# Kernel optimization log

Measured on AMD Instinct MI355X. Metric: run time of the kernel, lower is better.

## Reference

```python
import jax, jax.numpy as jnp
import numpy as np

EMBD = 256
HEAD = 4
HD = EMBD // HEAD  # 64
EPS = 1e-5


def setup_inputs() -> dict:
    key = jax.random.key(0)
    ks = jax.random.split(key, 12)
    s = lambda fan_in: 1.0 / np.sqrt(fan_in)
    return {
        "x": jax.random.normal(ks[0], (16, 1024, EMBD), dtype=jnp.float32),
        # attention params (stored as [in, out])
        "qkv_w": jax.random.uniform(ks[1], (EMBD, 3 * EMBD), jnp.float32, -s(EMBD), s(EMBD)),
        "qkv_b": jax.random.uniform(ks[2], (3 * EMBD,), jnp.float32, -s(EMBD), s(EMBD)),
        "out_w": jax.random.uniform(ks[3], (EMBD, EMBD), jnp.float32, -s(EMBD), s(EMBD)),
        "out_b": jax.random.uniform(ks[4], (EMBD,), jnp.float32, -s(EMBD), s(EMBD)),
        # MLP params
        "fc_w": jax.random.uniform(ks[5], (EMBD, 4 * EMBD), jnp.float32, -s(EMBD), s(EMBD)),
        "fc_b": jax.random.uniform(ks[6], (4 * EMBD,), jnp.float32, -s(EMBD), s(EMBD)),
        "proj_w": jax.random.uniform(ks[7], (4 * EMBD, EMBD), jnp.float32, -s(4 * EMBD), s(4 * EMBD)),
        "proj_b": jax.random.uniform(ks[8], (EMBD,), jnp.float32, -s(4 * EMBD), s(4 * EMBD)),
        # LayerNorm params
        "ln1_g": jnp.ones((EMBD,), jnp.float32),
        "ln1_b": jnp.zeros((EMBD,), jnp.float32),
        "ln2_g": jnp.ones((EMBD,), jnp.float32),
        "ln2_b": jnp.zeros((EMBD,), jnp.float32),
    }


def layer_norm(x, g, b):
    mu = jnp.mean(x, axis=-1, keepdims=True)
    var = jnp.mean(jnp.square(x - mu), axis=-1, keepdims=True)
    return (x - mu) * jax.lax.rsqrt(var + EPS) * g + b


def block_forward(x, qkv_w, qkv_b, out_w, out_b, fc_w, fc_b, proj_w, proj_b,
                  ln1_g, ln1_b, ln2_g, ln2_b):
    B, S, E = x.shape
    # --- attention branch ---
    h = layer_norm(x, ln1_g, ln1_b)
    qkv = h @ qkv_w + qkv_b                       # [B,S,3E]
    q, k, v = jnp.split(qkv, 3, axis=-1)
    q = q.reshape(B, S, HEAD, HD).transpose(0, 2, 1, 3)  # [B,H,S,D]
    k = k.reshape(B, S, HEAD, HD).transpose(0, 2, 1, 3)
    v = v.reshape(B, S, HEAD, HD).transpose(0, 2, 1, 3)
    att = jnp.einsum('bhqd,bhkd->bhqk', q, k) / jnp.sqrt(jnp.float32(HD))
    causal = jnp.tril(jnp.ones((S, S), dtype=bool))
    att = jnp.where(causal, att, -jnp.inf)
    att = jax.nn.softmax(att, axis=-1)
    o = jnp.einsum('bhqk,bhkd->bhqd', att, v)     # [B,H,S,D]
    o = o.transpose(0, 2, 1, 3).reshape(B, S, E)
    x = x + o @ out_w + out_b
    # --- MLP branch (dropout inactive at eval) ---
    h = layer_norm(x, ln2_g, ln2_b)
    h = jax.nn.relu(h @ fc_w + fc_b)
    x = x + h @ proj_w + proj_b
    return x


def reference(x, qkv_w, qkv_b, out_w, out_b, fc_w, fc_b, proj_w, proj_b,
              ln1_g, ln1_b, ln2_g, ln2_b):
    return block_forward(x, qkv_w, qkv_b, out_w, out_b, fc_w, fc_b,
                         proj_w, proj_b, ln1_g, ln1_b, ln2_g, ln2_b)
```

## Files before the change

### kernel.cpp

```cpp
#include <hip/hip_runtime.h>
#include <cstdint>


using f32x4  = __attribute__((ext_vector_type(4))) float;
using f32x16 = __attribute__((ext_vector_type(16))) float;
using s16x8  = __attribute__((ext_vector_type(8))) short;
using s16x4  = __attribute__((ext_vector_type(4))) short;

__device__ inline short f2bf(float f) {
    union { float f; unsigned u; } v{f};
    unsigned r = (v.u + 0x7FFFu + ((v.u >> 16) & 1u)) >> 16;
    return (short)r;
}

__device__ inline int cvt_pk_bf16(float lo, float hi) {
    int d;
    asm("v_cvt_pk_bf16_f32 %0, %1, %2" : "=v"(d) : "v"(lo), "v"(hi));
    return d;
}
__device__ inline void swap32(int& a, int& b) {
    asm("v_permlane32_swap_b32 %0, %1" : "+v"(a), "+v"(b));
}
__device__ inline void swap16(int& a, int& b) {
    asm("v_permlane16_swap_b32 %0, %1" : "+v"(a), "+v"(b));
}

__device__ inline void gload16(const void* g, void* l) {
    __builtin_amdgcn_global_load_lds(
        (const __attribute__((address_space(1))) void*)g,
        (__attribute__((address_space(3))) void*)l, 16, 0, 0);
}

__global__ __launch_bounds__(256) void prep_kernel(
    const float* __restrict__ qkv_w, const float* __restrict__ out_w,
    const float* __restrict__ fc_w,  const float* __restrict__ proj_w,
    short* __restrict__ wt_qkv, short* __restrict__ wt_out,
    short* __restrict__ wt_fc,  short* __restrict__ wt_proj,
    const float* __restrict__ x, const float* __restrict__ ln1_g,
    const float* __restrict__ ln1_b, short* __restrict__ hout)
{
    __shared__ short T[64][65];
    int id  = blockIdx.x;
    int tid = threadIdx.x;

    if (id < 192) {
        const float* W; short* Wt; int K, N, nt, kt;
        if (id < 48)       { W = qkv_w;  Wt = wt_qkv;  K = 256;  N = 768;  nt = id % 12;        kt = id / 12; }
        else if (id < 64)  { W = out_w;  Wt = wt_out;  K = 256;  N = 256;  nt = (id - 48) & 3;  kt = (id - 48) >> 2; }
        else if (id < 128) { W = fc_w;   Wt = wt_fc;   K = 256;  N = 1024; nt = (id - 64) & 15; kt = (id - 64) >> 4; }
        else               { W = proj_w; Wt = wt_proj; K = 1024; N = 256;  nt = (id - 128) & 3; kt = (id - 128) >> 2; }
        int n0 = nt * 64, k0 = kt * 64;
        int r = tid >> 2, c = (tid & 3) << 4;
        const float* src = W + (size_t)(k0 + r) * N + n0 + c;
#pragma unroll
        for (int u = 0; u < 4; ++u) {
            float4 v = *reinterpret_cast<const float4*>(src + u * 4);
            T[r][c + u * 4 + 0] = f2bf(v.x);
            T[r][c + u * 4 + 1] = f2bf(v.y);
            T[r][c + u * 4 + 2] = f2bf(v.z);
            T[r][c + u * 4 + 3] = f2bf(v.w);
        }
        __syncthreads();
        s16x8 o0, o1;
#pragma unroll
        for (int jj = 0; jj < 8; ++jj) { o0[jj] = T[c + jj][r]; o1[jj] = T[c + 8 + jj][r]; }
        short* dst = Wt + (size_t)(n0 + r) * K + k0 + c;
        *reinterpret_cast<s16x8*>(dst)     = o0;
        *reinterpret_cast<s16x8*>(dst + 8) = o1;
    } else {
        int lane = tid & 63;
        int row  = (id - 192) * 4 + (tid >> 6);
        const float* xr = x + (size_t)row * 256;
        float4 v = *reinterpret_cast<const float4*>(xr + lane * 4);
        float s = v.x + v.y + v.z + v.w;
#pragma unroll
        for (int o2 = 32; o2 >= 1; o2 >>= 1) s += __shfl_xor(s, o2);
        float mu = s * (1.0f / 256.0f);
        float dx = v.x - mu, dy = v.y - mu, dz = v.z - mu, dw = v.w - mu;
        float q = dx * dx + dy * dy + dz * dz + dw * dw;
#pragma unroll
        for (int o2 = 32; o2 >= 1; o2 >>= 1) q += __shfl_xor(q, o2);
        float rstd = rsqrtf(q * (1.0f / 256.0f) + 1e-5f);
        float4 gv = *reinterpret_cast<const float4*>(ln1_g + lane * 4);
        float4 bv = *reinterpret_cast<const float4*>(ln1_b + lane * 4);
        s16x4 ov;
        ov[0] = f2bf(dx * rstd * gv.x + bv.x);
        ov[1] = f2bf(dy * rstd * gv.y + bv.y);
        ov[2] = f2bf(dz * rstd * gv.z + bv.z);
        ov[3] = f2bf(dw * rstd * gv.w + bv.w);
        *reinterpret_cast<s16x4*>(hout + (size_t)row * 256 + lane * 4) = ov;
    }
}

template <int BM>
__global__ __launch_bounds__(256) void qkv_gemm_kernel(const short* __restrict__ A,
                                                       const short* __restrict__ Bt,
                                                       const float* __restrict__ bias,
                                                       short* __restrict__ qkout,
                                                       short* __restrict__ vt,
                                                       int N, int K)
{
    constexpr int MI = BM / 32;
    __shared__ short As[BM * 64];
    __shared__ short Bs[128 * 64];

    int tid = threadIdx.x;
    int l   = tid & 63;
    int w   = tid >> 6;
    int lr  = l & 15;
    int lk8 = (l >> 4) << 3;
    int r4  = (l >> 4) << 2;
    int wr  = w >> 1, wc = w & 1;
    int bn  = blockIdx.x * 128, bm = blockIdx.y * BM;

    int scolS = ((l & 7) << 3) ^ ((l >> 3) << 3);
    int srowA = w * (BM / 4) + (l >> 3);
    int srowB = (w << 5) + (l >> 3);
    const short* pa = A  + (size_t)(bm + srowA) * K + scolS;
    const short* pb = Bt + (size_t)(bn + srowB) * K + scolS;
    short* dstA = As + w * (BM / 4) * 64;
    short* dstB = Bs + (w << 11);

    f32x4 acc[MI][4];
#pragma unroll
    for (int mi = 0; mi < MI; ++mi)
#pragma unroll
        for (int ni = 0; ni < 4; ++ni) acc[mi][ni] = (f32x4){0.f, 0.f, 0.f, 0.f};

    int swz = (lr & 7) << 3;

    for (int k0 = 0; k0 < K; k0 += 64) {
        __syncthreads();
#pragma unroll
        for (int i = 0; i < BM / 32; ++i)
            gload16(pa + (size_t)(i * 8) * K + k0, dstA + (i << 9));
#pragma unroll
        for (int i = 0; i < 4; ++i)
            gload16(pb + (size_t)(i * 8) * K + k0, dstB + (i << 9));
        __syncthreads();

#pragma unroll
        for (int ks = 0; ks < 2; ++ks) {
            s16x8 af[MI], bf[4];
#pragma unroll
            for (int mi = 0; mi < MI; ++mi) {
                int row = wr * (BM / 2) + (mi << 4) + lr;
                af[mi] = *reinterpret_cast<const s16x8*>(
                    &As[(row << 6) + (((ks << 5) + lk8) ^ swz)]);
            }
#pragma unroll
            for (int ni = 0; ni < 4; ++ni) {
                int row = (wc << 6) + (ni << 4) + lr;
                bf[ni] = *reinterpret_cast<const s16x8*>(
                    &Bs[(row << 6) + (((ks << 5) + lk8) ^ swz)]);
            }
            __builtin_amdgcn_s_setprio(1);
#pragma unroll
            for (int mi = 0; mi < MI; ++mi)
#pragma unroll
                for (int ni = 0; ni < 4; ++ni)
                    acc[mi][ni] = __builtin_amdgcn_mfma_f32_16x16x32_bf16(
                        af[mi], bf[ni], acc[mi][ni], 0, 0, 0);
            __builtin_amdgcn_s_setprio(0);
        }
    }

    float bv[4];
#pragma unroll
    for (int ni = 0; ni < 4; ++ni)
        bv[ni] = bias[bn + (wc << 6) + (ni << 4) + lr];

#pragma unroll
    for (int mi = 0; mi < MI; ++mi) {
#pragma unroll
        for (int ni = 0; ni < 4; ++ni) {
            int n = bn + (wc << 6) + (ni << 4) + lr;
#pragma unroll
            for (int r = 0; r < 4; ++r) {
                int m = bm + wr * (BM / 2) + (mi << 4) + r4 + r;
                float v = acc[mi][ni][r] + bv[ni];
                if (bn < 512) {
                    qkout[(size_t)m * 512 + n] = f2bf(v);
                } else {
                    int hh = (n - 512) >> 6, dd = (n - 512) & 63;
                    int bb = m >> 10, ss = m & 1023;
                    vt[(size_t)((((bb << 2) | hh) << 6) | dd) * 1024 + ss] = f2bf(v);
                }
            }
        }
    }
}

__global__ __launch_bounds__(256) void oproj_ln_kernel(const short* __restrict__ A,
                                                       const short* __restrict__ Bt,
                                                       const float* __restrict__ bias,
                                                       const float* __restrict__ R,
                                                       float* __restrict__ x1,
                                                       short* __restrict__ h2,
                                                       const float* __restrict__ g,
                                                       const float* __restrict__ bb)
{
    constexpr int ASZ = 64 * 64;
    constexpr int BSZ = 256 * 64;
    __shared__ short As[2 * ASZ];
    __shared__ short Bs[2 * BSZ];

    int tid = threadIdx.x;
    int l   = tid & 63;
    int w   = tid >> 6;
    int lr  = l & 15;
    int lk8 = (l >> 4) << 3;
    int r4  = (l >> 4) << 2;
    int bm  = blockIdx.x * 64;

    int scolS = ((l & 7) << 3) ^ ((l >> 3) << 3);
    const short* pa = A  + (size_t)(bm + (w << 4) + (l >> 3)) * 256 + scolS;
    const short* pb = Bt + (size_t)((w << 6) + (l >> 3)) * 256 + scolS;
    short* dstA = As + (w << 10);
    short* dstB = Bs + (w << 12);

    f32x4 acc[16];
#pragma unroll
    for (int ni = 0; ni < 16; ++ni) acc[ni] = (f32x4){0.f, 0.f, 0.f, 0.f};

    int swz = (lr & 7) << 3;

#pragma unroll
    for (int i = 0; i < 2; ++i)
        gload16(pa + (size_t)(i * 8) * 256, dstA + (i << 9));
#pragma unroll
    for (int i = 0; i < 8; ++i)
        gload16(pb + (size_t)(i * 8) * 256, dstB + (i << 9));
    __syncthreads();

    int cur = 0;
    for (int k0 = 0; k0 < 256; k0 += 64) {
        if (k0 + 64 < 256) {
            int nxt = cur ^ 1;
#pragma unroll
            for (int i = 0; i < 2; ++i)
                gload16(pa + (size_t)(i * 8) * 256 + k0 + 64, dstA + nxt * ASZ + (i << 9));
#pragma unroll
            for (int i = 0; i < 8; ++i)
                gload16(pb + (size_t)(i * 8) * 256 + k0 + 64, dstB + nxt * BSZ + (i << 9));
        }
        const short* curA = As + cur * ASZ;
        const short* curB = Bs + cur * BSZ;
#pragma unroll
        for (int ks = 0; ks < 2; ++ks) {
            int arow = (w << 4) + lr;
            s16x8 af = *reinterpret_cast<const s16x8*>(
                &curA[(arow << 6) + (((ks << 5) + lk8) ^ swz)]);
            __builtin_amdgcn_s_setprio(1);
#pragma unroll
            for (int ni = 0; ni < 16; ++ni) {
                int row = (ni << 4) + lr;
                s16x8 bf = *reinterpret_cast<const s16x8*>(
                    &curB[(row << 6) + (((ks << 5) + lk8) ^ swz)]);
                acc[ni] = __builtin_amdgcn_mfma_f32_16x16x32_bf16(af, bf, acc[ni], 0, 0, 0);
            }
            __builtin_amdgcn_s_setprio(0);
        }
        __syncthreads();
        cur ^= 1;
    }

#pragma unroll
    for (int ni = 0; ni < 16; ++ni) {
        int n = (ni << 4) + lr;
        float bvx = bias[n];
#pragma unroll
        for (int r = 0; r < 4; ++r) {
            int m = bm + (w << 4) + r4 + r;
            acc[ni][r] += bvx + R[(size_t)m * 256 + n];
        }
    }
#pragma unroll
    for (int r = 0; r < 4; ++r) {
        float s = 0.0f;
#pragma unroll
        for (int ni = 0; ni < 16; ++ni) s += acc[ni][r];
        s += __shfl_xor(s, 1); s += __shfl_xor(s, 2);
        s += __shfl_xor(s, 4); s += __shfl_xor(s, 8);
        float mu = s * (1.0f / 256.0f);
        float q = 0.0f;
#pragma unroll
        for (int ni = 0; ni < 16; ++ni) {
            float d = acc[ni][r] - mu;
            q += d * d;
        }
        q += __shfl_xor(q, 1); q += __shfl_xor(q, 2);
        q += __shfl_xor(q, 4); q += __shfl_xor(q, 8);
        float rstd = rsqrtf(q * (1.0f / 256.0f) + 1e-5f);

        int m = bm + (w << 4) + r4 + r;
#pragma unroll
        for (int ni = 0; ni < 16; ++ni) {
            int n = (ni << 4) + lr;
            float v = acc[ni][r];
            x1[(size_t)m * 256 + n] = v;
            h2[(size_t)m * 256 + n] = f2bf((v - mu) * rstd * g[n] + bb[n]);
        }
    }
}

__global__ __launch_bounds__(256) void mlp_kernel(const short* __restrict__ h2,
                                                  const short* __restrict__ wfc,
                                                  const float* __restrict__ fcb,
                                                  const short* __restrict__ w2,
                                                  const float* __restrict__ pjb,
                                                  const float* __restrict__ x1,
                                                  float* __restrict__ out)
{
    __shared__ short H2s[4 * 64 * 64];
    __shared__ short WFCs[128 * 64];
    __shared__ short W2s[256 * 128];

    int tid = threadIdx.x;
    int l   = tid & 63;
    int w   = tid >> 6;
    int lr  = l & 15;
    int lk8 = (l >> 4) << 3;
    int r4  = (l >> 4) << 2;
    int bm  = blockIdx.x * 64;
    int swz = (lr & 7) << 3;

    int scolS = ((l & 7) << 3) ^ ((l >> 3) << 3);

    {
        const short* pa = h2 + (size_t)(bm + (w << 4) + (l >> 3)) * 256 + scolS;
#pragma unroll
        for (int ks4 = 0; ks4 < 4; ++ks4)
#pragma unroll
            for (int i = 0; i < 2; ++i)
                gload16(pa + (size_t)(i * 8) * 256 + ks4 * 64,
                        H2s + ks4 * 4096 + (w << 10) + (i << 9));
    }

    int srowB = (w << 5) + (l >> 3);
    const short* pwfc0 = wfc + (size_t)srowB * 256 + scolS;
    short* dstWFC = WFCs + (w << 11);
    int w2colS = ((l & 15) << 3) ^ ((((w << 2) + (l >> 4)) & 7) << 3);
    const short* pw2 = w2 + (size_t)((w << 2) + (l >> 4)) * 1024 + w2colS;
    short* dstW2 = W2s + (w << 9);

    f32x4 acc[16];
#pragma unroll
    for (int ni = 0; ni < 16; ++ni) acc[ni] = (f32x4){0.f, 0.f, 0.f, 0.f};

    for (int p = 0; p < 8; ++p) {
        const short* pwfc = pwfc0 + (size_t)(p * 128) * 256;

        f32x4 sv[8];
#pragma unroll
        for (int jt = 0; jt < 8; ++jt) sv[jt] = (f32x4){0.f, 0.f, 0.f, 0.f};

        for (int kstep = 0; kstep < 4; ++kstep) {
            __syncthreads();
#pragma unroll
            for (int i = 0; i < 4; ++i)
                gload16(pwfc + (size_t)(i * 8) * 256 + kstep * 64, dstWFC + (i << 9));
            __syncthreads();

#pragma unroll
            for (int ii = 0; ii < 4; ++ii) {
                int i = kstep * 4 + ii;
                gload16(pw2 + (size_t)(i * 16) * 1024 + p * 128, dstW2 + (i << 11));
            }

#pragma unroll
            for (int ks = 0; ks < 2; ++ks) {
                int qrow = (w << 4) + lr;
                s16x8 hf = *reinterpret_cast<const s16x8*>(
                    &H2s[kstep * 4096 + (qrow << 6) + (((ks << 5) + lk8) ^ swz)]);
                __builtin_amdgcn_s_setprio(1);
#pragma unroll
                for (int jt = 0; jt < 8; ++jt) {
                    int row = (jt << 4) + lr;
                    s16x8 wf = *reinterpret_cast<const s16x8*>(
                        &WFCs[(row << 6) + (((ks << 5) + lk8) ^ swz)]);
                    sv[jt] = __builtin_amdgcn_mfma_f32_16x16x32_bf16(wf, hf, sv[jt], 0, 0, 0);
                }
                __builtin_amdgcn_s_setprio(0);
            }
        }

#pragma unroll
        for (int jt = 0; jt < 8; ++jt) {
            float4 fb = *reinterpret_cast<const float4*>(fcb + p * 128 + jt * 16 + r4);
            sv[jt][0] = fmaxf(sv[jt][0] + fb.x, 0.0f);
            sv[jt][1] = fmaxf(sv[jt][1] + fb.y, 0.0f);
            sv[jt][2] = fmaxf(sv[jt][2] + fb.z, 0.0f);
            sv[jt][3] = fmaxf(sv[jt][3] + fb.w, 0.0f);
        }

        int cpk[8][2];
#pragma unroll
        for (int jt = 0; jt < 8; ++jt) {
            cpk[jt][0] = cvt_pk_bf16(sv[jt][0], sv[jt][1]);
            cpk[jt][1] = cvt_pk_bf16(sv[jt][2], sv[jt][3]);
        }

        __syncthreads();

#pragma unroll
        for (int ks2 = 0; ks2 < 4; ++ks2) {
            int a0 = cpk[2 * ks2][0],     a1 = cpk[2 * ks2][1];
            int b0 = cpk[2 * ks2 + 1][0], b1 = cpk[2 * ks2 + 1][1];
            swap32(a0, b0); swap32(a1, b1);
            swap16(a0, b0); swap16(a1, b1);
            union { int i[4]; s16x8 v; } fr;
            fr.i[0] = a0; fr.i[1] = a1; fr.i[2] = b0; fr.i[3] = b1;
            __builtin_amdgcn_s_setprio(1);
#pragma unroll
            for (int ni = 0; ni < 16; ++ni) {
                int row = (ni << 4) + lr;
                s16x8 w2f = *reinterpret_cast<const s16x8*>(
                    &W2s[(row << 7) + (((ks2 << 5) + lk8) ^ swz)]);
                acc[ni] = __builtin_amdgcn_mfma_f32_16x16x32_bf16(fr.v, w2f, acc[ni], 0, 0, 0);
            }
            __builtin_amdgcn_s_setprio(0);
        }
    }

#pragma unroll
    for (int ni = 0; ni < 16; ++ni) {
        int n = (ni << 4) + lr;
        float bvx = pjb[n];
#pragma unroll
        for (int r = 0; r < 4; ++r) {
            int m = bm + (w << 4) + r4 + r;
            out[(size_t)m * 256 + n] = acc[ni][r] + bvx + x1[(size_t)m * 256 + n];
        }
    }
}

__global__ __launch_bounds__(256, 2) void attn_kernel(const short* __restrict__ qk,
                                                      const short* __restrict__ vt,
                                                      short* __restrict__ o)
{
    constexpr int KSZ = 128 * 64;
    constexpr int VSZ = 64 * 128;
    __shared__ short Ks[2 * KSZ];
    __shared__ short Vs[2 * VSZ];

    int bid  = blockIdx.x;
    int xcd  = bid & 7;
    int j    = bid >> 3;
    int bhg  = j & 7;
    int qidx = j >> 3;
    int qt   = qidx < 4 ? qidx : 11 - qidx;
    int bh   = (bhg << 3) | xcd;
    int b = bh >> 2, h = bh & 3;

    int tid = threadIdx.x;
    int l   = tid & 63;
    int w   = tid >> 6;
    int lq  = l & 31;
    int hg  = l >> 5;

    int krow0 = (w << 3) + (l >> 3);
    int kscol = ((l & 7) << 3) ^ (((l >> 3) & 7) << 3);
    const short* kgp = qk + (size_t)(b * 1024 + krow0) * 512 + 256 + h * 64 + kscol;
    short* dstK = Ks + (w << 3) * 64;
    int vrow0 = (w << 2) + (l >> 4);
    int vscol = ((l & 15) << 3) ^ ((vrow0 & 7) << 3);
    const short* vgp = vt + (size_t)((bh << 6) + vrow0) * 1024 + vscol;
    short* dstV = Vs + (w << 2) * 128;

    const float SC = 0.125f * 1.44269504088896f;

    const short* qrow = qk + (size_t)(b * 1024 + qt * 128 + (w << 5) + lq) * 512
                        + h * 64 + (hg << 3);
    s16x8 qf[4];
#pragma unroll
    for (int ds = 0; ds < 4; ++ds)
        qf[ds] = *reinterpret_cast<const s16x8*>(qrow + 16 * ds);

#pragma unroll
    for (int i = 0; i < 4; ++i) {
        gload16(kgp + (size_t)(i * 32) * 512, dstK + i * 32 * 64);
        gload16(vgp + (size_t)(i * 16) * 1024, dstV + i * 16 * 128);
    }
    __syncthreads();

    float m = -1e30f, lsum = 0.0f;
    f32x16 oacc[2];
#pragma unroll
    for (int dt = 0; dt < 2; ++dt)
#pragma unroll
        for (int r = 0; r < 16; ++r) oacc[dt][r] = 0.0f;
    int qglob = qt * 128 + (w << 5) + lq;
    int cur = 0;
    int niter = qt + 1;

    for (int kt = 0; kt < niter; ++kt) {
        if (kt + 1 < niter) {
            int nxt = cur ^ 1;
#pragma unroll
            for (int i = 0; i < 4; ++i) {
                gload16(kgp + (size_t)((kt + 1) * 128 + i * 32) * 512,
                        dstK + nxt * KSZ + i * 32 * 64);
                gload16(vgp + (size_t)(i * 16) * 1024 + (kt + 1) * 128,
                        dstV + nxt * VSZ + i * 16 * 128);
            }
        }

        f32x16 sv[4];
#pragma unroll
        for (int jt = 0; jt < 4; ++jt)
#pragma unroll
            for (int r = 0; r < 16; ++r) sv[jt][r] = 0.0f;
        __builtin_amdgcn_s_setprio(1);
#pragma unroll
        for (int ds = 0; ds < 4; ++ds) {
#pragma unroll
            for (int jt = 0; jt < 4; ++jt) {
                int row = jt * 32 + lq;
                s16x8 kf = *reinterpret_cast<const s16x8*>(
                    &Ks[cur * KSZ + (row << 6) + ((16 * ds + (hg << 3)) ^ ((row & 7) << 3))]);
                sv[jt] = __builtin_amdgcn_mfma_f32_32x32x16_bf16(kf, qf[ds], sv[jt], 0, 0, 0);
            }
        }
        __builtin_amdgcn_s_setprio(0);
#pragma unroll
        for (int jt = 0; jt < 4; ++jt)
#pragma unroll
            for (int r = 0; r < 16; ++r) sv[jt][r] *= SC;

        if (kt == niter - 1) {
#pragma unroll
            for (int jt = 0; jt < 4; ++jt)
#pragma unroll
                for (int r = 0; r < 16; ++r) {
                    int kg = kt * 128 + jt * 32 + (r & 3) + ((r >> 2) << 3) + (hg << 2);
                    if (kg > qglob) sv[jt][r] = -1e30f;
                }
        }

        float rm = -1e30f;
#pragma unroll
        for (int jt = 0; jt < 4; ++jt)
#pragma unroll
            for (int r = 0; r < 16; ++r) rm = fmaxf(rm, sv[jt][r]);
        rm = fmaxf(rm, __shfl_xor(rm, 32));
        bool big = __any(rm > m + 8.0f);
        float fct = 1.0f;
        if (big) {
            float mn = fmaxf(m, rm);
            fct = exp2f(m - mn);
            m = mn;
        }
        float ps = 0.0f;
#pragma unroll
        for (int jt = 0; jt < 4; ++jt)
#pragma unroll
            for (int r = 0; r < 16; ++r) {
                float p = exp2f(sv[jt][r] - m);
                sv[jt][r] = p;
                ps += p;
            }
        ps += __shfl_xor(ps, 32);
        lsum = lsum * fct + ps;

        if (big) {
#pragma unroll
            for (int r = 0; r < 16; ++r) {
                float f = __shfl(fct, (r & 3) + ((r >> 2) << 3) + (hg << 2));
                oacc[0][r] *= f;
                oacc[1][r] *= f;
            }
        }

#pragma unroll
        for (int jt = 0; jt < 4; ++jt) {
            int x0 = cvt_pk_bf16(sv[jt][0],  sv[jt][1]);
            int x1v = cvt_pk_bf16(sv[jt][2],  sv[jt][3]);
            int y0 = cvt_pk_bf16(sv[jt][4],  sv[jt][5]);
            int y1 = cvt_pk_bf16(sv[jt][6],  sv[jt][7]);
            int z0 = cvt_pk_bf16(sv[jt][8],  sv[jt][9]);
            int z1 = cvt_pk_bf16(sv[jt][10], sv[jt][11]);
            int w0 = cvt_pk_bf16(sv[jt][12], sv[jt][13]);
            int w1 = cvt_pk_bf16(sv[jt][14], sv[jt][15]);
            swap32(x0, y0); swap32(x1v, y1);
            swap32(z0, w0); swap32(z1, w1);
            union { int i[4]; s16x8 v; } fA, fB;
            fA.i[0] = x0; fA.i[1] = x1v; fA.i[2] = y0; fA.i[3] = y1;
            fB.i[0] = z0; fB.i[1] = z1;  fB.i[2] = w0; fB.i[3] = w1;
            __builtin_amdgcn_s_setprio(1);
#pragma unroll
            for (int dt = 0; dt < 2; ++dt) {
                int row = dt * 32 + lq;
                int rs  = (row & 7) << 3;
                s16x8 vfA = *reinterpret_cast<const s16x8*>(
                    &Vs[cur * VSZ + (row << 7) + ((16 * (2 * jt)     + (hg << 3)) ^ rs)]);
                oacc[dt] = __builtin_amdgcn_mfma_f32_32x32x16_bf16(fA.v, vfA, oacc[dt], 0, 0, 0);
                s16x8 vfB = *reinterpret_cast<const s16x8*>(
                    &Vs[cur * VSZ + (row << 7) + ((16 * (2 * jt + 1) + (hg << 3)) ^ rs)]);
                oacc[dt] = __builtin_amdgcn_mfma_f32_32x32x16_bf16(fB.v, vfB, oacc[dt], 0, 0, 0);
            }
            __builtin_amdgcn_s_setprio(0);
        }

        if (kt + 1 < niter) {
            __syncthreads();
            cur ^= 1;
        }
    }

#pragma unroll
    for (int r = 0; r < 16; ++r) {
        int qr  = (r & 3) + ((r >> 2) << 3) + (hg << 2);
        float lv  = __shfl(lsum, qr);
        float inv = 1.0f / lv;
        int q = qt * 128 + (w << 5) + qr;
        short* orow = o + (size_t)(b * 1024 + q) * 256 + h * 64;
        orow[lq]      = f2bf(oacc[0][r] * inv);
        orow[32 + lq] = f2bf(oacc[1][r] * inv);
    }
}

extern "C" void kernel_launch(void* const* d_in, const int* in_sizes, int n_in,
                              void* d_out, int out_size, void* d_ws, size_t ws_size,
                              hipStream_t stream)
{
    const float* x      = (const float*)d_in[0];
    const float* qkv_w  = (const float*)d_in[1];
    const float* qkv_b  = (const float*)d_in[2];
    const float* out_w  = (const float*)d_in[3];
    const float* out_b  = (const float*)d_in[4];
    const float* fc_w   = (const float*)d_in[5];
    const float* fc_b   = (const float*)d_in[6];
    const float* proj_w = (const float*)d_in[7];
    const float* proj_b = (const float*)d_in[8];
    const float* ln1_g  = (const float*)d_in[9];
    const float* ln1_b  = (const float*)d_in[10];
    const float* ln2_g  = (const float*)d_in[11];
    const float* ln2_b  = (const float*)d_in[12];
    float* out = (float*)d_out;

    short* ws = (short*)d_ws;
    short* wt_qkv  = ws;
    short* wt_out  = ws + 196608;
    short* wt_fc   = ws + 262144;
    short* wt_proj = ws + 524288;
    short* bufA    = ws + 786432;
    short* qk_buf  = ws + 4980736;
    short* vt_buf  = ws + 13369344;

    dim3 blk(256);

    prep_kernel<<<dim3(4288), blk, 0, stream>>>(
        qkv_w, out_w, fc_w, proj_w, wt_qkv, wt_out, wt_fc, wt_proj,
        x, ln1_g, ln1_b, bufA);
    qkv_gemm_kernel<128><<<dim3(6, 128), blk, 0, stream>>>(
        bufA, wt_qkv, qkv_b, qk_buf, vt_buf, 768, 256);
    attn_kernel<<<dim3(512), blk, 0, stream>>>(qk_buf, vt_buf, bufA);
    oproj_ln_kernel<<<dim3(256), blk, 0, stream>>>(
        bufA, wt_out, out_b, x, out, bufA, ln2_g, ln2_b);
    mlp_kernel<<<dim3(256), blk, 0, stream>>>(
        bufA, wt_fc, fc_b, wt_proj, proj_b, out, out);
}
```

Measured before the change: 127.8 us.

## Restructure MLP kernel into 64-wide hidden chunks with prefetched weight tiles

The fused MLP kernel now walks the 1024-wide hidden dimension in 16 chunks of 64 instead of 8 chunks of 128. Each chunk loads the full-K slice of the fc weights at once rather than in four k-steps. The proj weight tile is double-buffered, and the next chunk's fc and proj weights are prefetched while the current chunk's second GEMM runs. This removes the per-k-step barrier pairs and hides global-to-LDS load latency behind MFMA work, at the cost of more chunk iterations and a slightly larger LDS footprint.

```diff
diff --git a/kernel.cpp b/kernel.cpp
--- a/kernel.cpp
+++ b/kernel.cpp
@@ -313,8 +313,8 @@
                                                   float* __restrict__ out)
 {
     __shared__ short H2s[4 * 64 * 64];
-    __shared__ short WFCs[128 * 64];
-    __shared__ short W2s[256 * 128];
+    __shared__ short WFCs[64 * 256];
+    __shared__ short W2s[2 * 256 * 64];
 
     int tid = threadIdx.x;
     int l   = tid & 63;
@@ -325,9 +325,8 @@
     int bm  = blockIdx.x * 64;
     int swz = (lr & 7) << 3;
 
-    int scolS = ((l & 7) << 3) ^ ((l >> 3) << 3);
-
     {
+        int scolS = ((l & 7) << 3) ^ ((l >> 3) << 3);
         const short* pa = h2 + (size_t)(bm + (w << 4) + (l >> 3)) * 256 + scolS;
 #pragma unroll
         for (int ks4 = 0; ks4 < 4; ++ks4)
@@ -337,74 +336,77 @@
                         H2s + ks4 * 4096 + (w << 10) + (i << 9));
     }
 
-    int srowB = (w << 5) + (l >> 3);
-    const short* pwfc0 = wfc + (size_t)srowB * 256 + scolS;
-    short* dstWFC = WFCs + (w << 11);
-    int w2colS = ((l & 15) << 3) ^ ((((w << 2) + (l >> 4)) & 7) << 3);
-    const short* pw2 = w2 + (size_t)((w << 2) + (l >> 4)) * 1024 + w2colS;
+    int fr0  = (w << 1) + (l >> 5);
+    int fcol = ((l & 31) << 3) ^ ((fr0 & 7) << 3);
+    const short* pwfc = wfc + (size_t)fr0 * 256 + fcol;
+    short* dstWFC = WFCs + (w << 9);
+
+    int wr0  = (w << 3) + (l >> 3);
+    int wcol = ((l & 7) << 3) ^ (((l >> 3) & 7) << 3);
+    const short* pw2 = w2 + (size_t)wr0 * 1024 + wcol;
     short* dstW2 = W2s + (w << 9);
 
     f32x4 acc[16];
 #pragma unroll
     for (int ni = 0; ni < 16; ++ni) acc[ni] = (f32x4){0.f, 0.f, 0.f, 0.f};
 
-    for (int p = 0; p < 8; ++p) {
-        const short* pwfc = pwfc0 + (size_t)(p * 128) * 256;
-
-        f32x4 sv[8];
-#pragma unroll
-        for (int jt = 0; jt < 8; ++jt) sv[jt] = (f32x4){0.f, 0.f, 0.f, 0.f};
-
-        for (int kstep = 0; kstep < 4; ++kstep) {
-            __syncthreads();
-#pragma unroll
-            for (int i = 0; i < 4; ++i)
-                gload16(pwfc + (size_t)(i * 8) * 256 + kstep * 64, dstWFC + (i << 9));
-            __syncthreads();
-
-#pragma unroll
-            for (int ii = 0; ii < 4; ++ii) {
-                int i = kstep * 4 + ii;
-                gload16(pw2 + (size_t)(i * 16) * 1024 + p * 128, dstW2 + (i << 11));
-            }
-
-#pragma unroll
-            for (int ks = 0; ks < 2; ++ks) {
-                int qrow = (w << 4) + lr;
-                s16x8 hf = *reinterpret_cast<const s16x8*>(
-                    &H2s[kstep * 4096 + (qrow << 6) + (((ks << 5) + lk8) ^ swz)]);
-                __builtin_amdgcn_s_setprio(1);
-#pragma unroll
-                for (int jt = 0; jt < 8; ++jt) {
-                    int row = (jt << 4) + lr;
-                    s16x8 wf = *reinterpret_cast<const s16x8*>(
-                        &WFCs[(row << 6) + (((ks << 5) + lk8) ^ swz)]);
-                    sv[jt] = __builtin_amdgcn_mfma_f32_16x16x32_bf16(wf, hf, sv[jt], 0, 0, 0);
-                }
-                __builtin_amdgcn_s_setprio(0);
-            }
-        }
-
-#pragma unroll
-        for (int jt = 0; jt < 8; ++jt) {
-            float4 fb = *reinterpret_cast<const float4*>(fcb + p * 128 + jt * 16 + r4);
-            sv[jt][0] = fmaxf(sv[jt][0] + fb.x, 0.0f);
-            sv[jt][1] = fmaxf(sv[jt][1] + fb.y, 0.0f);
-            sv[jt][2] = fmaxf(sv[jt][2] + fb.z, 0.0f);
-            sv[jt][3] = fmaxf(sv[jt][3] + fb.w, 0.0f);
-        }
-
-        int cpk[8][2];
-#pragma unroll
-        for (int jt = 0; jt < 8; ++jt) {
-            cpk[jt][0] = cvt_pk_bf16(sv[jt][0], sv[jt][1]);
-            cpk[jt][1] = cvt_pk_bf16(sv[jt][2], sv[jt][3]);
-        }
-
+#pragma unroll
+    for (int i = 0; i < 8; ++i) {
+        gload16(pwfc + (size_t)(i * 8) * 256, dstWFC + (i << 11));
+        gload16(pw2 + (size_t)(i * 32) * 1024, dstW2 + (i << 11));
+    }
+
+    int buf = 0;
+    for (int p = 0; p < 16; ++p) {
         __syncthreads();
 
-#pragma unroll
-        for (int ks2 = 0; ks2 < 4; ++ks2) {
+        f32x4 sv[4];
+#pragma unroll
+        for (int jt = 0; jt < 4; ++jt) sv[jt] = (f32x4){0.f, 0.f, 0.f, 0.f};
+#pragma unroll
+        for (int ksg = 0; ksg < 8; ++ksg) {
+            int qrow = (w << 4) + lr;
+            s16x8 hf = *reinterpret_cast<const s16x8*>(
+                &H2s[(ksg >> 1) * 4096 + (qrow << 6) + ((((ksg & 1) << 5) + lk8) ^ swz)]);
+            __builtin_amdgcn_s_setprio(1);
+#pragma unroll
+            for (int jt = 0; jt < 4; ++jt) {
+                int row = (jt << 4) + lr;
+                s16x8 wf = *reinterpret_cast<const s16x8*>(
+                    &WFCs[(row << 8) + (((ksg << 5) + lk8) ^ swz)]);
+                sv[jt] = __builtin_amdgcn_mfma_f32_16x16x32_bf16(wf, hf, sv[jt], 0, 0, 0);
+            }
+            __builtin_amdgcn_s_setprio(0);
+        }
+
+        int cpk[4][2];
+#pragma unroll
+        for (int jt = 0; jt < 4; ++jt) {
+            float4 fb = *reinterpret_cast<const float4*>(fcb + p * 64 + jt * 16 + r4);
+            float v0 = fmaxf(sv[jt][0] + fb.x, 0.0f);
+            float v1 = fmaxf(sv[jt][1] + fb.y, 0.0f);
+            float v2 = fmaxf(sv[jt][2] + fb.z, 0.0f);
+            float v3 = fmaxf(sv[jt][3] + fb.w, 0.0f);
+            cpk[jt][0] = cvt_pk_bf16(v0, v1);
+            cpk[jt][1] = cvt_pk_bf16(v2, v3);
+        }
+
+        __syncthreads();
+
+        if (p < 15) {
+            const short* pf = pwfc + (size_t)(p + 1) * 64 * 256;
+            const short* p2 = pw2 + (p + 1) * 64;
+            short* d2 = dstW2 + (buf ^ 1) * 16384;
+#pragma unroll
+            for (int i = 0; i < 8; ++i) {
+                gload16(pf + (size_t)(i * 8) * 256, dstWFC + (i << 11));
+                gload16(p2 + (size_t)(i * 32) * 1024, d2 + (i << 11));
+            }
+        }
+
+        const short* W2cur = W2s + buf * 16384;
+#pragma unroll
+        for (int ks2 = 0; ks2 < 2; ++ks2) {
             int a0 = cpk[2 * ks2][0],     a1 = cpk[2 * ks2][1];
             int b0 = cpk[2 * ks2 + 1][0], b1 = cpk[2 * ks2 + 1][1];
             swap32(a0, b0); swap32(a1, b1);
@@ -416,11 +418,12 @@
             for (int ni = 0; ni < 16; ++ni) {
                 int row = (ni << 4) + lr;
                 s16x8 w2f = *reinterpret_cast<const s16x8*>(
-                    &W2s[(row << 7) + (((ks2 << 5) + lk8) ^ swz)]);
+                    &W2cur[(row << 6) + (((ks2 << 5) + lk8) ^ swz)]);
                 acc[ni] = __builtin_amdgcn_mfma_f32_16x16x32_bf16(fr.v, w2f, acc[ni], 0, 0, 0);
             }
             __builtin_amdgcn_s_setprio(0);
         }
+        buf ^= 1;
     }
 
 #pragma unroll
```

New measurement: 126.6 us. No clear change (-0.9%).
